# Optimization experiments

Measured on AMD Instinct MI355X. Metric: run time of the kernel, lower is better.

The kernel has to match this reference:

```python
import jax, jax.numpy as jnp
import numpy as np

WZ, WH, WW = 2, 6, 12          # window_size
NW = 64                        # type_of_windows = (8//2)*(96//6)
HEADS = 12
DIM = 384
B_ = 15                        # batch(1) * num_lon_windows(180//12)
N = WZ * WH * WW               # 144 tokens per window


def _construct_position_index():
    zi = np.arange(WZ); zj = -np.arange(WZ) * WZ
    hi = np.arange(WH); hj = -np.arange(WH) * WH
    w = np.arange(WW)
    c1 = np.stack(np.meshgrid(zi, hi, w, indexing='ij')).reshape(3, -1)
    c2 = np.stack(np.meshgrid(zj, hj, w, indexing='ij')).reshape(3, -1)
    coords = (c1[:, :, None] - c2[:, None, :]).transpose(1, 2, 0)  # (N, N, 3)
    coords[..., 2] += WW - 1
    coords[..., 1] *= 2 * WW - 1
    coords[..., 0] *= (2 * WW - 1) * WH * WH
    return coords.sum(-1).reshape(-1).astype(np.int32)  # (N*N,)


def setup_inputs() -> dict:
    key = jax.random.key(0)
    ks = jax.random.split(key, 6)
    bias_rows = (2 * WW - 1) * WH * WH * WZ * WZ  # 3312
    return {
        'x': jax.random.normal(ks[0], (B_, NW, N, DIM), dtype=jnp.float32),
        'mask': jnp.zeros((B_, N, N), dtype=jnp.float32),
        'w_qkv': jax.random.normal(ks[1], (DIM, 3 * DIM), dtype=jnp.float32) * 0.02,
        'b_qkv': jnp.zeros((3 * DIM,), dtype=jnp.float32),
        'w_proj': jax.random.normal(ks[2], (DIM, DIM), dtype=jnp.float32) * 0.02,
        'b_proj': jnp.zeros((DIM,), dtype=jnp.float32),
        'bias_table': jax.random.normal(ks[3], (bias_rows, NW, HEADS), dtype=jnp.float32) * 0.02,
        'position_index': jnp.asarray(_construct_position_index()),
    }


def reference(x, mask, w_qkv, b_qkv, w_proj, b_proj, bias_table, position_index):
    b_, nw, n, c = x.shape
    hd = c // HEADS
    scale = hd ** -0.5
    qkv = (x @ w_qkv + b_qkv).reshape(b_, nw, n, 3, HEADS, hd)
    q, k, v = jnp.moveaxis(qkv, 3, 0)            # each (B_, nW, N, H, hd)
    attn = jnp.einsum('bwnhd,bwmhd->bwhnm', q * scale, k)  # (B_, nW, H, N, N)
    # earth-specific relative bias gather: (N*N, nW, H) -> (nW, H, N, N)
    bias = bias_table[position_index].reshape(n, n, nw, HEADS).transpose(2, 3, 0, 1)
    attn = attn + bias[None]                     # broadcast over B_
    attn = attn + mask[:, None, None, :, :]      # additive mask per lon window
    attn = jax.nn.softmax(attn, axis=-1)         # dropout_rate=0 -> identity
    out = jnp.einsum('bwhnm,bwmhd->bwnhd', attn, v).reshape(b_, nw, n, c)
    return out @ w_proj + b_proj
```

## Files before the change

### kernel.cpp

```cpp
#include <hip/hip_runtime.h>
#include <cstdint>


typedef _Float16 f16;
typedef _Float16 f16x8 __attribute__((ext_vector_type(8)));
typedef _Float16 f16x4v __attribute__((ext_vector_type(4)));
typedef float f32x4 __attribute__((ext_vector_type(4)));

#define NW_ 64
#define HEADS_ 12
#define DIM_ 384
#define BATCH_ 15
#define NTOK_ 144
#define HD_ 32
#define MTOK_ (BATCH_*NW_*NTOK_)
#define NWH_ (BATCH_*NW_*HEADS_)
#define NMSQ_ (NTOK_*NTOK_)

__device__ __forceinline__ void load16_lds(const void* g, void* l) {
    __builtin_amdgcn_global_load_lds(
        (const __attribute__((address_space(1))) uint32_t*)g,
        (__attribute__((address_space(3))) uint32_t*)l,
        16, 0, 0);
}

__device__ __forceinline__ f32x4 fzero4() {
    f32x4 z; z[0]=0.f; z[1]=0.f; z[2]=0.f; z[3]=0.f; return z;
}

__global__ void cvt_f32_to_f16(const float* __restrict__ src, f16* __restrict__ dst, int n4) {
    int i = blockIdx.x * blockDim.x + threadIdx.x;
    int stride = gridDim.x * blockDim.x;
    for (; i < n4; i += stride) {
        float4 v = ((const float4*)src)[i];
        f16x4v o;
        o[0] = (f16)v.x; o[1] = (f16)v.y; o[2] = (f16)v.z; o[3] = (f16)v.w;
        *(f16x4v*)(dst + 4*(size_t)i) = o;
    }
}

__global__ void transpose_cvt(const float* __restrict__ src, f16* __restrict__ dst, int K, int N) {
    int i = blockIdx.x * blockDim.x + threadIdx.x;
    if (i >= K*N) return;
    int n = i / K;
    int k = i - n*K;
    dst[i] = (f16)src[k*N + n];
}

__global__ __launch_bounds__(256) void bias_gather(
    const float* __restrict__ bias_table, const int* __restrict__ pos_idx,
    float* __restrict__ dense)
{
    int wh = blockIdx.x;
    int nm = blockIdx.y * 256 + threadIdx.x;
    int idx = pos_idx[nm];
    dense[(size_t)wh*NMSQ_ + nm] = bias_table[(size_t)idx*(NW_*HEADS_) + wh];
}

__global__ __launch_bounds__(256) void qkv_gemm(
    const f16* __restrict__ A, const f16* __restrict__ Bt,
    const float* __restrict__ bias,
    f16* __restrict__ qws, f16* __restrict__ kws, f16* __restrict__ vws)
{
    constexpr int BK = 32;
    constexpr int NT = DIM_/BK;
    __shared__ __align__(16) f16 Asm[2][128*BK];
    __shared__ __align__(16) f16 Bsm[2][128*BK];
    const int tid  = threadIdx.x;
    const int lane = tid & 63;
    const int wave = tid >> 6;
    const int l15  = lane & 15;
    const int quad = lane >> 4;
    const int wr = wave >> 1, wc = wave & 1;

    unsigned lin = blockIdx.x;
    lin = (lin & 7u) * 1215u + (lin >> 3);
    const int row0 = (int)(lin / 9u) * 128;
    const int col0 = (int)(lin % 9u) * 128;

    f32x4 acc[4][4];
    #pragma unroll
    for (int i = 0; i < 4; ++i)
        #pragma unroll
        for (int j = 0; j < 4; ++j) acc[i][j] = fzero4();

    auto stage = [&](int kt, int b) {
        const int k0 = kt * BK;
        #pragma unroll
        for (int cc = 0; cc < 2; ++cc) {
            int chunk  = wave*2 + cc;
            int flat16 = chunk*64 + lane;
            int r   = flat16 >> 2;
            int c16 = flat16 & 3;
            load16_lds(&A [(size_t)(row0 + r)*DIM_ + k0 + c16*8], (char*)(&Asm[b][0]) + chunk*1024);
            load16_lds(&Bt[(size_t)(col0 + r)*DIM_ + k0 + c16*8], (char*)(&Bsm[b][0]) + chunk*1024);
        }
    };
    auto compute = [&](int b) {
        f16x8 af[4], bf[4];
        #pragma unroll
        for (int i = 0; i < 4; ++i)
            af[i] = *(const f16x8*)&Asm[b][(wr*64 + i*16 + l15)*BK + quad*8];
        #pragma unroll
        for (int j = 0; j < 4; ++j)
            bf[j] = *(const f16x8*)&Bsm[b][(wc*64 + j*16 + l15)*BK + quad*8];
        #pragma unroll
        for (int i = 0; i < 4; ++i)
            #pragma unroll
            for (int j = 0; j < 4; ++j)
                acc[i][j] = __builtin_amdgcn_mfma_f32_16x16x32_f16(af[i], bf[j], acc[i][j], 0, 0, 0);
    };

    stage(0, 0);
    asm volatile("s_waitcnt vmcnt(0)" ::: "memory");
    __builtin_amdgcn_s_barrier();
    __builtin_amdgcn_sched_barrier(0);
    int cur = 0;
    for (int kt = 0; kt < NT-1; ++kt) {
        stage(kt+1, cur^1);
        compute(cur);
        asm volatile("s_waitcnt vmcnt(0) lgkmcnt(0)" ::: "memory");
        __builtin_amdgcn_s_barrier();
        __builtin_amdgcn_sched_barrier(0);
        cur ^= 1;
    }
    compute(cur);

    const int which = col0 / DIM_;
    #pragma unroll
    for (int j = 0; j < 4; ++j) {
        int col = col0 + wc*64 + j*16 + l15;
        float bq = bias[col];
        int rem = col - which*DIM_;
        int h = rem >> 5, d = rem & 31;
        #pragma unroll
        for (int i = 0; i < 4; ++i) {
            int rowb = row0 + wr*64 + i*16 + quad*4;
            #pragma unroll
            for (int r = 0; r < 4; ++r) {
                int row = rowb + r;
                int bw  = row / NTOK_;
                int n   = row - bw*NTOK_;
                int head = bw*HEADS_ + h;
                f16 hv = (f16)(acc[i][j][r] + bq);
                if (which == 0)      qws[(size_t)head*NTOK_*HD_ + n*HD_ + d] = hv;
                else if (which == 1) kws[(size_t)head*NTOK_*HD_ + n*HD_ + d] = hv;
                else                 vws[(size_t)head*HD_*NTOK_ + d*NTOK_ + n] = hv;
            }
        }
    }
}

__global__ __launch_bounds__(576) void attention(
    const f16* __restrict__ qws, const f16* __restrict__ kws, const f16* __restrict__ vws,
    const float* __restrict__ bias_dense,
    const float* __restrict__ mask, f16* __restrict__ ows)
{
    constexpr int KPAD = 40;
    constexpr int VPAD = 168;
    __shared__ __align__(16) char smem[10752 + 48384];
    f16* Vt  = (f16*)smem;
    f16* Ksm = (f16*)(smem + 10752);
    f16* Pst = (f16*)(smem + 10752);

    const int tid  = threadIdx.x;
    const int lane = tid & 63;
    const int wv   = tid >> 6;
    const int l15  = lane & 15;
    const int quad = lane >> 4;

    unsigned bid = blockIdx.x;
    unsigned lin = (bid & 7u) * 1440u + (bid >> 3);
    const int wh = (int)(lin / 15u);
    const int b  = (int)(lin - (unsigned)wh*15u);
    const int w  = wh / HEADS_;
    const int h  = wh - w*HEADS_;

    const int bwh = b*(NW_*HEADS_) + wh;
    const f16* qh = qws + (size_t)bwh*NTOK_*HD_;
    const f16* kh = kws + (size_t)bwh*NTOK_*HD_;
    const f16* vh = vws + (size_t)bwh*HD_*NTOK_;

    if (tid < 64) {
        int d = tid >> 1, m0 = 144 + (tid & 1)*8;
        uint4 z = {0u,0u,0u,0u};
        *(uint4*)&Vt[d*VPAD + m0] = z;
    }

    {
        int flat = tid*8;
        int n = flat >> 5, d = flat & 31;
        *(uint4*)&Ksm[n*KPAD + d] = *(const uint4*)&kh[flat];
        int dv = flat / NTOK_;
        int mv = flat - dv*NTOK_;
        *(uint4*)&Vt[dv*VPAD + mv] = *(const uint4*)&vh[flat];
    }
    const int nq = wv*16 + l15;
    f16x8 qf = *(const f16x8*)&qh[nq*HD_ + quad*8];

    const float* bd = bias_dense + (size_t)wh*NMSQ_;
    float brg[9][4];
    #pragma unroll
    for (int j = 0; j < 9; ++j) {
        int m = j*16 + l15;
        #pragma unroll
        for (int r = 0; r < 4; ++r)
            brg[j][r] = bd[(wv*16 + quad*4 + r)*NTOK_ + m];
    }

    __syncthreads();

    f32x4 sfr[9];
    #pragma unroll
    for (int j = 0; j < 9; ++j) {
        f16x8 kf = *(const f16x8*)&Ksm[(j*16 + l15)*KPAD + quad*8];
        sfr[j] = __builtin_amdgcn_mfma_f32_16x16x32_f16(qf, kf, fzero4(), 0, 0, 0);
    }
    __syncthreads();

    const float scale = 0.17677669529663687f;

    float p[9][4], rmax[4], rsum[4];
    #pragma unroll
    for (int r = 0; r < 4; ++r) rmax[r] = -1e30f;
    const float* mrow = mask + (size_t)b*NMSQ_;
    #pragma unroll
    for (int j = 0; j < 9; ++j) {
        int m = j*16 + l15;
        #pragma unroll
        for (int r = 0; r < 4; ++r) {
            int n = wv*16 + quad*4 + r;
            float s = sfr[j][r]*scale + brg[j][r] + mrow[n*NTOK_ + m];
            p[j][r] = s;
            rmax[r] = fmaxf(rmax[r], s);
        }
    }
    #pragma unroll
    for (int r = 0; r < 4; ++r) {
        float v = rmax[r];
        #pragma unroll
        for (int off = 1; off < 16; off <<= 1)
            v = fmaxf(v, __shfl_xor(v, off, 64));
        rmax[r] = v;
    }
    #pragma unroll
    for (int r = 0; r < 4; ++r) rsum[r] = 0.f;
    #pragma unroll
    for (int j = 0; j < 9; ++j)
        #pragma unroll
        for (int r = 0; r < 4; ++r) {
            float e = __expf(p[j][r] - rmax[r]);
            p[j][r] = e;
            rsum[r] += e;
        }
    #pragma unroll
    for (int r = 0; r < 4; ++r) {
        float v = rsum[r];
        #pragma unroll
        for (int off = 1; off < 16; off <<= 1)
            v += __shfl_xor(v, off, 64);
        rsum[r] = 1.0f / v;
    }

    f16* Pw = Pst + wv*16*VPAD;
    #pragma unroll
    for (int j = 0; j < 9; ++j) {
        int m = j*16 + l15;
        #pragma unroll
        for (int r = 0; r < 4; ++r)
            Pw[(quad*4 + r)*VPAD + m] = (f16)p[j][r];
    }
    if (lane < 32) {
        int row = lane >> 1, m0 = 144 + (lane & 1)*8;
        uint4 z = {0u,0u,0u,0u};
        *(uint4*)&Pw[row*VPAD + m0] = z;
    }

    f32x4 o0 = fzero4(), o1 = fzero4();
    #pragma unroll
    for (int s = 0; s < 5; ++s) {
        f16x8 pa = *(const f16x8*)&Pw[l15*VPAD + s*32 + quad*8];
        f16x8 v0 = *(const f16x8*)&Vt[l15*VPAD + s*32 + quad*8];
        f16x8 v1 = *(const f16x8*)&Vt[(16 + l15)*VPAD + s*32 + quad*8];
        o0 = __builtin_amdgcn_mfma_f32_16x16x32_f16(pa, v0, o0, 0, 0, 0);
        o1 = __builtin_amdgcn_mfma_f32_16x16x32_f16(pa, v1, o1, 0, 0, 0);
    }

    const int bw = b*NW_ + w;
    #pragma unroll
    for (int r = 0; r < 4; ++r) {
        int n = wv*16 + quad*4 + r;
        size_t base = ((size_t)bw*NTOK_ + n)*DIM_ + h*HD_;
        ows[base + l15]      = (f16)(o0[r]*rsum[r]);
        ows[base + 16 + l15] = (f16)(o1[r]*rsum[r]);
    }
}

__global__ __launch_bounds__(256) void proj_gemm(
    const f16* __restrict__ A, const f16* __restrict__ Bt,
    const float* __restrict__ bias, float* __restrict__ out)
{
    constexpr int BK = 32;
    constexpr int NT = DIM_/BK;
    __shared__ __align__(16) f16 Asm[2][128*BK];
    __shared__ __align__(16) f16 Bsm[2][128*BK];
    const int tid  = threadIdx.x;
    const int lane = tid & 63;
    const int wave = tid >> 6;
    const int l15  = lane & 15;
    const int quad = lane >> 4;
    const int wr = wave >> 1, wc = wave & 1;

    unsigned lin = blockIdx.x;
    lin = (lin & 7u) * 405u + (lin >> 3);
    const int row0 = (int)(lin / 3u) * 128;
    const int col0 = (int)(lin % 3u) * 128;

    f32x4 acc[4][4];
    #pragma unroll
    for (int i = 0; i < 4; ++i)
        #pragma unroll
        for (int j = 0; j < 4; ++j) acc[i][j] = fzero4();

    auto stage = [&](int kt, int b) {
        const int k0 = kt * BK;
        #pragma unroll
        for (int cc = 0; cc < 2; ++cc) {
            int chunk  = wave*2 + cc;
            int flat16 = chunk*64 + lane;
            int r   = flat16 >> 2;
            int c16 = flat16 & 3;
            load16_lds(&A [(size_t)(row0 + r)*DIM_ + k0 + c16*8], (char*)(&Asm[b][0]) + chunk*1024);
            load16_lds(&Bt[(size_t)(col0 + r)*DIM_ + k0 + c16*8], (char*)(&Bsm[b][0]) + chunk*1024);
        }
    };
    auto compute = [&](int b) {
        f16x8 af[4], bf[4];
        #pragma unroll
        for (int i = 0; i < 4; ++i)
            af[i] = *(const f16x8*)&Asm[b][(wr*64 + i*16 + l15)*BK + quad*8];
        #pragma unroll
        for (int j = 0; j < 4; ++j)
            bf[j] = *(const f16x8*)&Bsm[b][(wc*64 + j*16 + l15)*BK + quad*8];
        #pragma unroll
        for (int i = 0; i < 4; ++i)
            #pragma unroll
            for (int j = 0; j < 4; ++j)
                acc[i][j] = __builtin_amdgcn_mfma_f32_16x16x32_f16(af[i], bf[j], acc[i][j], 0, 0, 0);
    };

    stage(0, 0);
    asm volatile("s_waitcnt vmcnt(0)" ::: "memory");
    __builtin_amdgcn_s_barrier();
    __builtin_amdgcn_sched_barrier(0);
    int cur = 0;
    for (int kt = 0; kt < NT-1; ++kt) {
        stage(kt+1, cur^1);
        compute(cur);
        asm volatile("s_waitcnt vmcnt(0) lgkmcnt(0)" ::: "memory");
        __builtin_amdgcn_s_barrier();
        __builtin_amdgcn_sched_barrier(0);
        cur ^= 1;
    }
    compute(cur);

    #pragma unroll
    for (int j = 0; j < 4; ++j) {
        int col = col0 + wc*64 + j*16 + l15;
        float bp = bias[col];
        #pragma unroll
        for (int i = 0; i < 4; ++i) {
            int rowb = row0 + wr*64 + i*16 + quad*4;
            #pragma unroll
            for (int r = 0; r < 4; ++r)
                out[(size_t)(rowb + r)*DIM_ + col] = acc[i][j][r] + bp;
        }
    }
}

extern "C" void kernel_launch(void* const* d_in, const int* in_sizes, int n_in,
                              void* d_out, int out_size, void* d_ws, size_t ws_size,
                              hipStream_t stream)
{
    const float* x      = (const float*)d_in[0];
    const float* mask   = (const float*)d_in[1];
    const float* w_qkv  = (const float*)d_in[2];
    const float* b_qkv  = (const float*)d_in[3];
    const float* w_proj = (const float*)d_in[4];
    const float* b_proj = (const float*)d_in[5];
    const float* btab   = (const float*)d_in[6];
    const int*   pidx   = (const int*)d_in[7];
    float* out = (float*)d_out;

    constexpr size_t X16_B = (size_t)MTOK_*DIM_*2;
    constexpr size_t WTQ_B = (size_t)1152*384*2;
    constexpr size_t WTP_B = (size_t)384*384*2;
    constexpr size_t HEAD_B = (size_t)NWH_*NTOK_*HD_*2;

    char* ws = (char*)d_ws;
    f16* x16 = (f16*)ws;
    f16* wtq = (f16*)(ws + X16_B);
    f16* wtp = (f16*)(ws + X16_B + WTQ_B);
    f16* qws = (f16*)(ws + X16_B + WTQ_B + WTP_B);
    f16* kws = (f16*)((char*)qws + HEAD_B);
    f16* vws = (f16*)((char*)kws + HEAD_B);
    f16* ows = x16;

    float* bias_dense = (float*)d_out;

    cvt_f32_to_f16<<<8192, 256, 0, stream>>>(x, x16, MTOK_*DIM_/4);
    transpose_cvt<<<(384*1152 + 255)/256, 256, 0, stream>>>(w_qkv, wtq, 384, 1152);
    transpose_cvt<<<(384*384  + 255)/256, 256, 0, stream>>>(w_proj, wtp, 384, 384);
    bias_gather<<<dim3(NW_*HEADS_, NMSQ_/256), 256, 0, stream>>>(btab, pidx, bias_dense);
    qkv_gemm<<<9720, 256, 0, stream>>>(x16, wtq, b_qkv, qws, kws, vws);
    attention<<<NWH_, 576, 0, stream>>>(qws, kws, vws, bias_dense, mask, ows);
    proj_gemm<<<3240, 256, 0, stream>>>(ows, wtp, b_proj, out);
}
```

Baseline: 1.043 ms.

## Triple-buffer GEMM LDS staging and XOR-swizzle tiles to avoid bank conflicts

Both the QKV and projection GEMMs move from double to triple buffering in LDS. Each keeps two stages in flight and waits with vmcnt(4) instead of draining all loads before each step. The 16-byte chunk column inside each LDS row is also XOR-swizzled by row, on both the global-to-LDS copy and the fragment reads, to cut bank conflicts on the ds_read of f16x8 fragments. This adds LDS use, which may lower occupancy, in exchange for deeper load/compute overlap.

```diff
diff --git a/kernel.cpp b/kernel.cpp
--- a/kernel.cpp
+++ b/kernel.cpp
@@ -64,8 +64,8 @@
 {
     constexpr int BK = 32;
     constexpr int NT = DIM_/BK;
-    __shared__ __align__(16) f16 Asm[2][128*BK];
-    __shared__ __align__(16) f16 Bsm[2][128*BK];
+    __shared__ __align__(16) f16 Asm[3][128*BK];
+    __shared__ __align__(16) f16 Bsm[3][128*BK];
     const int tid  = threadIdx.x;
     const int lane = tid & 63;
     const int wave = tid >> 6;
@@ -92,18 +92,25 @@
             int flat16 = chunk*64 + lane;
             int r   = flat16 >> 2;
             int c16 = flat16 & 3;
-            load16_lds(&A [(size_t)(row0 + r)*DIM_ + k0 + c16*8], (char*)(&Asm[b][0]) + chunk*1024);
-            load16_lds(&Bt[(size_t)(col0 + r)*DIM_ + k0 + c16*8], (char*)(&Bsm[b][0]) + chunk*1024);
+            int cs  = c16 ^ ((r >> 1) & 3);
+            load16_lds(&A [(size_t)(row0 + r)*DIM_ + k0 + cs*8], (char*)(&Asm[b][0]) + chunk*1024);
+            load16_lds(&Bt[(size_t)(col0 + r)*DIM_ + k0 + cs*8], (char*)(&Bsm[b][0]) + chunk*1024);
         }
     };
     auto compute = [&](int b) {
         f16x8 af[4], bf[4];
         #pragma unroll
-        for (int i = 0; i < 4; ++i)
-            af[i] = *(const f16x8*)&Asm[b][(wr*64 + i*16 + l15)*BK + quad*8];
-        #pragma unroll
-        for (int j = 0; j < 4; ++j)
-            bf[j] = *(const f16x8*)&Bsm[b][(wc*64 + j*16 + l15)*BK + quad*8];
+        for (int i = 0; i < 4; ++i) {
+            int row = wr*64 + i*16 + l15;
+            int s   = quad ^ ((row >> 1) & 3);
+            af[i] = *(const f16x8*)&Asm[b][row*BK + s*8];
+        }
+        #pragma unroll
+        for (int j = 0; j < 4; ++j) {
+            int row = wc*64 + j*16 + l15;
+            int s   = quad ^ ((row >> 1) & 3);
+            bf[j] = *(const f16x8*)&Bsm[b][row*BK + s*8];
+        }
         #pragma unroll
         for (int i = 0; i < 4; ++i)
             #pragma unroll
@@ -112,19 +119,23 @@
     };
 
     stage(0, 0);
-    asm volatile("s_waitcnt vmcnt(0)" ::: "memory");
+    stage(1, 1);
+    #pragma unroll
+    for (int kt = 0; kt < NT-2; ++kt) {
+        asm volatile("s_waitcnt vmcnt(4) lgkmcnt(0)" ::: "memory");
+        __builtin_amdgcn_s_barrier();
+        __builtin_amdgcn_sched_barrier(0);
+        stage(kt+2, (kt+2)%3);
+        compute(kt%3);
+    }
+    asm volatile("s_waitcnt vmcnt(4) lgkmcnt(0)" ::: "memory");
     __builtin_amdgcn_s_barrier();
     __builtin_amdgcn_sched_barrier(0);
-    int cur = 0;
-    for (int kt = 0; kt < NT-1; ++kt) {
-        stage(kt+1, cur^1);
-        compute(cur);
-        asm volatile("s_waitcnt vmcnt(0) lgkmcnt(0)" ::: "memory");
-        __builtin_amdgcn_s_barrier();
-        __builtin_amdgcn_sched_barrier(0);
-        cur ^= 1;
-    }
-    compute(cur);
+    compute((NT-2)%3);
+    asm volatile("s_waitcnt vmcnt(0) lgkmcnt(0)" ::: "memory");
+    __builtin_amdgcn_s_barrier();
+    __builtin_amdgcn_sched_barrier(0);
+    compute((NT-1)%3);
 
     const int which = col0 / DIM_;
     #pragma unroll
@@ -302,8 +313,8 @@
 {
     constexpr int BK = 32;
     constexpr int NT = DIM_/BK;
-    __shared__ __align__(16) f16 Asm[2][128*BK];
-    __shared__ __align__(16) f16 Bsm[2][128*BK];
+    __shared__ __align__(16) f16 Asm[3][128*BK];
+    __shared__ __align__(16) f16 Bsm[3][128*BK];
     const int tid  = threadIdx.x;
     const int lane = tid & 63;
     const int wave = tid >> 6;
@@ -330,18 +341,25 @@
             int flat16 = chunk*64 + lane;
             int r   = flat16 >> 2;
             int c16 = flat16 & 3;
-            load16_lds(&A [(size_t)(row0 + r)*DIM_ + k0 + c16*8], (char*)(&Asm[b][0]) + chunk*1024);
-            load16_lds(&Bt[(size_t)(col0 + r)*DIM_ + k0 + c16*8], (char*)(&Bsm[b][0]) + chunk*1024);
+            int cs  = c16 ^ ((r >> 1) & 3);
+            load16_lds(&A [(size_t)(row0 + r)*DIM_ + k0 + cs*8], (char*)(&Asm[b][0]) + chunk*1024);
+            load16_lds(&Bt[(size_t)(col0 + r)*DIM_ + k0 + cs*8], (char*)(&Bsm[b][0]) + chunk*1024);
         }
     };
     auto compute = [&](int b) {
         f16x8 af[4], bf[4];
         #pragma unroll
-        for (int i = 0; i < 4; ++i)
-            af[i] = *(const f16x8*)&Asm[b][(wr*64 + i*16 + l15)*BK + quad*8];
-        #pragma unroll
-        for (int j = 0; j < 4; ++j)
-            bf[j] = *(const f16x8*)&Bsm[b][(wc*64 + j*16 + l15)*BK + quad*8];
+        for (int i = 0; i < 4; ++i) {
+            int row = wr*64 + i*16 + l15;
+            int s   = quad ^ ((row >> 1) & 3);
+            af[i] = *(const f16x8*)&Asm[b][row*BK + s*8];
+        }
+        #pragma unroll
+        for (int j = 0; j < 4; ++j) {
+            int row = wc*64 + j*16 + l15;
+            int s   = quad ^ ((row >> 1) & 3);
+            bf[j] = *(const f16x8*)&Bsm[b][row*BK + s*8];
+        }
         #pragma unroll
         for (int i = 0; i < 4; ++i)
             #pragma unroll
@@ -350,19 +368,23 @@
     };
 
     stage(0, 0);
-    asm volatile("s_waitcnt vmcnt(0)" ::: "memory");
+    stage(1, 1);
+    #pragma unroll
+    for (int kt = 0; kt < NT-2; ++kt) {
+        asm volatile("s_waitcnt vmcnt(4) lgkmcnt(0)" ::: "memory");
+        __builtin_amdgcn_s_barrier();
+        __builtin_amdgcn_sched_barrier(0);
+        stage(kt+2, (kt+2)%3);
+        compute(kt%3);
+    }
+    asm volatile("s_waitcnt vmcnt(4) lgkmcnt(0)" ::: "memory");
     __builtin_amdgcn_s_barrier();
     __builtin_amdgcn_sched_barrier(0);
-    int cur = 0;
-    for (int kt = 0; kt < NT-1; ++kt) {
-        stage(kt+1, cur^1);
-        compute(cur);
-        asm volatile("s_waitcnt vmcnt(0) lgkmcnt(0)" ::: "memory");
-        __builtin_amdgcn_s_barrier();
-        __builtin_amdgcn_sched_barrier(0);
-        cur ^= 1;
-    }
-    compute(cur);
+    compute((NT-2)%3);
+    asm volatile("s_waitcnt vmcnt(0) lgkmcnt(0)" ::: "memory");
+    __builtin_amdgcn_s_barrier();
+    __builtin_amdgcn_sched_barrier(0);
+    compute((NT-1)%3);
 
     #pragma unroll
     for (int j = 0; j < 4; ++j) {
```

Result: no change. 1.035 ms (-0.8%).
